# Kernel tuning notes

Hardware: AMD Instinct MI355X
Metric: run time of the kernel (lower is better)

## Reference

```python
import jax, jax.numpy as jnp
import numpy as np

D = 1024      # model_dim
H = 16        # num_attention_heads
HD = D // H   # head dim
FFN = 4096    # ffn_dim
EPS = 1e-5


def _mha(q_in, k_in, v_in, wq, bq, wk, bk, wv, bv):
    B, Sq, _ = q_in.shape
    Sk = k_in.shape[1]
    def split(x, S):
        return x.reshape(B, S, H, HD).transpose(0, 2, 1, 3)  # [B,H,S,HD]
    Q = split(q_in @ wq + bq, Sq)
    K = split(k_in @ wk + bk, Sk)
    V = split(v_in @ wv + bv, Sk)
    scores = jnp.einsum('bhqd,bhkd->bhqk', Q, K) / (HD ** 0.5)
    probs = jax.nn.softmax(scores, axis=-1)
    ctx = jnp.einsum('bhqk,bhkd->bhqd', probs, V)
    return ctx.transpose(0, 2, 1, 3).reshape(B, Sq, D)


def _ln(x, g, b):
    mu = jnp.mean(x, axis=-1, keepdims=True)
    var = jnp.mean(jnp.square(x - mu), axis=-1, keepdims=True)
    return (x - mu) * jax.lax.rsqrt(var + EPS) * g + b


def setup_inputs() -> dict:
    key = jax.random.key(0)
    ks = jax.random.split(key, 24)
    s = 1.0 / np.sqrt(D)
    inp = {
        'hidden_states': jax.random.normal(ks[0], (2, 2048, D), jnp.float32),
        'encoder_hidden_states': jax.random.normal(ks[1], (2, 2048, D), jnp.float32),
        # self-attention projections
        'sa_wq': jax.random.normal(ks[2], (D, D), jnp.float32) * s,
        'sa_bq': jnp.zeros((D,), jnp.float32),
        'sa_wk': jax.random.normal(ks[3], (D, D), jnp.float32) * s,
        'sa_bk': jnp.zeros((D,), jnp.float32),
        'sa_wv': jax.random.normal(ks[4], (D, D), jnp.float32) * s,
        'sa_bv': jnp.zeros((D,), jnp.float32),
        'ln1_g': jnp.ones((D,), jnp.float32),
        'ln1_b': jnp.zeros((D,), jnp.float32),
        # cross-attention projections
        'ca_wq': jax.random.normal(ks[5], (D, D), jnp.float32) * s,
        'ca_bq': jnp.zeros((D,), jnp.float32),
        'ca_wk': jax.random.normal(ks[6], (D, D), jnp.float32) * s,
        'ca_bk': jnp.zeros((D,), jnp.float32),
        'ca_wv': jax.random.normal(ks[7], (D, D), jnp.float32) * s,
        'ca_bv': jnp.zeros((D,), jnp.float32),
        'ln2_g': jnp.ones((D,), jnp.float32),
        'ln2_b': jnp.zeros((D,), jnp.float32),
        # feed-forward
        'fc1_w': jax.random.normal(ks[8], (D, FFN), jnp.float32) * s,
        'fc1_b': jnp.zeros((FFN,), jnp.float32),
        'fc2_w': jax.random.normal(ks[9], (FFN, D), jnp.float32) * (1.0 / np.sqrt(FFN)),
        'fc2_b': jnp.zeros((D,), jnp.float32),
        'ln3_g': jnp.ones((D,), jnp.float32),
        'ln3_b': jnp.zeros((D,), jnp.float32),
    }
    return inp


def reference(hidden_states, encoder_hidden_states,
              sa_wq, sa_bq, sa_wk, sa_bk, sa_wv, sa_bv, ln1_g, ln1_b,
              ca_wq, ca_bq, ca_wk, ca_bk, ca_wv, ca_bv, ln2_g, ln2_b,
              fc1_w, fc1_b, fc2_w, fc2_b, ln3_g, ln3_b):
    # self-attention + residual + LN  (dropout = identity in eval)
    h = _mha(hidden_states, hidden_states, hidden_states,
             sa_wq, sa_bq, sa_wk, sa_bk, sa_wv, sa_bv)
    x = _ln(hidden_states + h, ln1_g, ln1_b)
    # cross-attention + residual + LN
    h = _mha(x, encoder_hidden_states, encoder_hidden_states,
             ca_wq, ca_bq, ca_wk, ca_bk, ca_wv, ca_bv)
    x = _ln(x + h, ln2_g, ln2_b)
    # feed-forward + residual + LN
    h = jax.nn.relu(x @ fc1_w + fc1_b) @ fc2_w + fc2_b
    return _ln(x + h, ln3_g, ln3_b)
```

## Files before the change

kernel.cpp:

```cpp
#include <hip/hip_runtime.h>


typedef unsigned short u16;
typedef short v8s __attribute__((ext_vector_type(8)));
typedef float v4f __attribute__((ext_vector_type(4)));

#define LDP 72
#define LOG2E 1.44269504088896340736f

__device__ __forceinline__ float b2f(u16 h) {
    return __uint_as_float(((unsigned)h) << 16);
}
__device__ __forceinline__ u16 f2b(float f) {
    unsigned u = __float_as_uint(f);
    u += 0x7fffu + ((u >> 16) & 1u);
    return (u16)(u >> 16);
}
__device__ __forceinline__ u16 f2b_rz(float f) {
    return (u16)(__float_as_uint(f) >> 16);
}
__device__ __forceinline__ v8s pack8(const float* p) {
    float4 f0 = *(const float4*)p;
    float4 f1 = *(const float4*)(p + 4);
    v8s r;
    r[0] = (short)f2b(f0.x); r[1] = (short)f2b(f0.y);
    r[2] = (short)f2b(f0.z); r[3] = (short)f2b(f0.w);
    r[4] = (short)f2b(f1.x); r[5] = (short)f2b(f1.y);
    r[6] = (short)f2b(f1.z); r[7] = (short)f2b(f1.w);
    return r;
}
__device__ __forceinline__ void gload16(const void* g, void* l) {
    __builtin_amdgcn_global_load_lds(
        (const __attribute__((address_space(1))) unsigned int*)g,
        (__attribute__((address_space(3))) unsigned int*)l, 16, 0, 0);
}

__global__ __launch_bounds__(256) void transpose_f2b(
    const float* __restrict__ src, u16* __restrict__ dst, int R, int C)
{
    __shared__ u16 tile[32][33];
    const int t  = threadIdx.x;
    const int tx = t & 31, ty = t >> 5;
    const int r0 = blockIdx.y * 32, c0 = blockIdx.x * 32;
#pragma unroll
    for (int i = 0; i < 32; i += 8)
        tile[ty + i][tx] = f2b(src[(size_t)(r0 + ty + i) * C + c0 + tx]);
    __syncthreads();
#pragma unroll
    for (int i = 0; i < 32; i += 8)
        dst[(size_t)(c0 + ty + i) * R + r0 + tx] = tile[tx][ty + i];
}

__global__ __launch_bounds__(256) void prep_bias(
    const float* __restrict__ bq, const float* __restrict__ bk, const float* __restrict__ bv,
    const float* __restrict__ cbk, const float* __restrict__ cbv,
    float* __restrict__ sab, float* __restrict__ cakvb)
{
    int i = blockIdx.x * 256 + threadIdx.x;
    if (i < 1024) {
        sab[i]          = bq[i];
        sab[1024 + i]   = bk[i];
        sab[2048 + i]   = bv[i];
        cakvb[i]        = cbk[i];
        cakvb[1024 + i] = cbv[i];
    }
}

template <int AF32, int BN>
__global__ __launch_bounds__(256) void gemm_bt(
    const void* __restrict__ Ap, const u16* __restrict__ Bt,
    const float* __restrict__ bias, u16* __restrict__ C,
    int M, int N, int K, int relu, int qcols, float qscale,
    u16* __restrict__ vt, int vtcol0)
{
    constexpr int NI = BN / 32;
    __shared__ __align__(16) u16 Al[128 * 64];
    __shared__ __align__(16) u16 Bl[BN * 64];
    const int tid  = threadIdx.x;
    const int wave = tid >> 6, lane = tid & 63;
    const int quad = lane >> 4, tl = lane & 15;
    const int bm0 = blockIdx.y * 128, bn0 = blockIdx.x * BN;
    const int wm = (wave >> 1) * 64, wn = (wave & 1) * (BN / 2);
    const int srow = lane >> 3;
    const int scol = (((lane & 7) ^ srow) << 3);

    const v4f z4 = {0.f, 0.f, 0.f, 0.f};
    v4f acc[4][NI];
#pragma unroll
    for (int i = 0; i < 4; ++i)
#pragma unroll
        for (int j = 0; j < NI; ++j) acc[i][j] = z4;

    for (int kt = 0; kt < K; kt += 64) {
#pragma unroll
        for (int i = 0; i < 4; ++i) {
            const int c = wave * 4 + i;
            const int row = c * 8 + srow;
            if (AF32) {
                const float* Af = (const float*)Ap;
                *(v8s*)&Al[(size_t)row * 64 + scol] =
                    pack8(&Af[(size_t)(bm0 + row) * K + kt + ((lane & 7) << 3)]);
            } else {
                const u16* Ab = (const u16*)Ap;
                gload16(&Ab[(size_t)(bm0 + row) * K + kt + scol], &Al[c * 512]);
            }
        }
#pragma unroll
        for (int i = 0; i < NI; ++i) {
            const int c = wave * NI + i;
            const int row = c * 8 + srow;
            gload16(&Bt[(size_t)(bn0 + row) * K + kt + scol], &Bl[c * 512]);
        }
        __syncthreads();
#pragma unroll
        for (int kk = 0; kk < 2; ++kk) {
            const int pc = ((kk * 4 + quad) ^ (tl & 7)) << 3;
            v8s af[4], bf[NI];
#pragma unroll
            for (int i = 0; i < 4; ++i) af[i] = *(const v8s*)&Al[(wm + i * 16 + tl) * 64 + pc];
#pragma unroll
            for (int i = 0; i < NI; ++i) bf[i] = *(const v8s*)&Bl[(wn + i * 16 + tl) * 64 + pc];
#pragma unroll
            for (int mi = 0; mi < 4; ++mi)
#pragma unroll
                for (int ni = 0; ni < NI; ++ni)
                    acc[mi][ni] = __builtin_amdgcn_mfma_f32_16x16x32_bf16(
                        af[mi], bf[ni], acc[mi][ni], 0, 0, 0);
        }
        __syncthreads();
    }
#pragma unroll
    for (int ni = 0; ni < NI; ++ni) {
        int col = bn0 + wn + ni * 16 + tl;
        float bv = bias[col];
        if (vtcol0 >= 0 && col >= vtcol0) {
            int cv = col - vtcol0;
            int h = cv >> 6, hd = cv & 63;
#pragma unroll
            for (int mi = 0; mi < 4; ++mi) {
                int row0 = bm0 + wm + mi * 16 + (quad << 2);
                int bb = row0 >> 11, s = row0 & 2047;
                ushort4 pk;
                pk.x = f2b(acc[mi][ni][0] + bv);
                pk.y = f2b(acc[mi][ni][1] + bv);
                pk.z = f2b(acc[mi][ni][2] + bv);
                pk.w = f2b(acc[mi][ni][3] + bv);
                *(ushort4*)&vt[((size_t)(bb * 16 + h) * 64 + hd) * 2048 + s] = pk;
            }
        } else {
            float sc = (col < qcols) ? qscale : 1.0f;
#pragma unroll
            for (int mi = 0; mi < 4; ++mi) {
                int row0 = bm0 + wm + mi * 16 + (quad << 2);
#pragma unroll
                for (int r = 0; r < 4; ++r) {
                    float vv = acc[mi][ni][r] + bv;
                    if (relu) vv = fmaxf(vv, 0.f);
                    vv *= sc;
                    C[(size_t)(row0 + r) * N + col] = f2b(vv);
                }
            }
        }
    }
}

__global__ __launch_bounds__(256) void attn_v5(
    const u16* __restrict__ Q, int qs, const u16* __restrict__ Kp, int ks,
    const u16* __restrict__ Vt, u16* __restrict__ O, int os, int Sk)
{
    __shared__ __align__(16) u16 Kl[128 * 64];
    __shared__ __align__(16) u16 Vtl[64 * 128];
    __shared__ __align__(16) u16 Pl[4][32 * LDP];

    const int tid  = threadIdx.x;
    const int wave = tid >> 6, lane = tid & 63;
    const int quad = lane >> 4, tl = lane & 15;
    const int b = blockIdx.y >> 4, h = blockIdx.y & 15;
    const int srow = lane >> 3;
    const int scolK = (((lane & 7) ^ srow) << 3);
    const int vri = lane >> 4, vj = lane & 15;

    const u16* qb  = Q  + (size_t)(b * 2048) * qs + h * 64;
    const u16* kb  = Kp + (size_t)(b * 2048) * ks + h * 64;
    const u16* vtb = Vt + (size_t)blockIdx.y * 64 * 2048;
    u16*       ob  = O  + (size_t)(b * 2048) * os + h * 64;
    const int qr0 = blockIdx.x * 128 + wave * 32;

    v8s qf[2][2];
#pragma unroll
    for (int mi = 0; mi < 2; ++mi)
#pragma unroll
        for (int kk = 0; kk < 2; ++kk)
            qf[mi][kk] = *(const v8s*)&qb[(size_t)(qr0 + mi * 16 + tl) * qs + kk * 32 + quad * 8];

    const v4f z4 = {0.f, 0.f, 0.f, 0.f};
    v4f oacc[2][4] = {{z4, z4, z4, z4}, {z4, z4, z4, z4}};
    float l_part[2][4] = {{0.f, 0.f, 0.f, 0.f}, {0.f, 0.f, 0.f, 0.f}};
    u16* Pw = &Pl[wave][0];

    const int pc0 = (quad ^ (tl & 7)) << 3;
    const int pc1 = ((4 + quad) ^ (tl & 7)) << 3;

    for (int kt = 0; kt < Sk; kt += 128) {
#pragma unroll
        for (int i = 0; i < 4; ++i) {
            const int c = wave * 4 + i;
            const int row = c * 8 + srow;
            gload16(&kb[(size_t)(kt + row) * ks + scolK], &Kl[c * 512]);
        }
#pragma unroll
        for (int i = 0; i < 4; ++i) {
            const int c = wave * 4 + i;
            const int vr = c * 4 + vri;
            const int g = (vj & 8) | ((vj & 7) ^ (vr & 7));
            gload16(&vtb[(size_t)vr * 2048 + kt + (g << 3)], &Vtl[c * 512]);
        }
        __syncthreads();

#pragma unroll
        for (int hf = 0; hf < 2; ++hf) {
#pragma unroll
            for (int nt = 0; nt < 4; ++nt) {
                const int krow = ((hf * 4 + nt) * 16 + tl) * 64;
                v8s k0 = *(const v8s*)&Kl[krow + pc0];
                v8s k1 = *(const v8s*)&Kl[krow + pc1];
#pragma unroll
                for (int mi = 0; mi < 2; ++mi) {
                    v4f a = z4;
                    a = __builtin_amdgcn_mfma_f32_16x16x32_bf16(qf[mi][0], k0, a, 0, 0, 0);
                    a = __builtin_amdgcn_mfma_f32_16x16x32_bf16(qf[mi][1], k1, a, 0, 0, 0);
#pragma unroll
                    for (int r = 0; r < 4; ++r) {
                        float p = exp2f(a[r]);
                        l_part[mi][r] += p;
                        Pw[(mi * 16 + quad * 4 + r) * LDP + nt * 16 + tl] = f2b_rz(p);
                    }
                }
            }
            asm volatile("" ::: "memory");

            v8s pf[2][2];
#pragma unroll
            for (int mi = 0; mi < 2; ++mi) {
                pf[mi][0] = *(const v8s*)&Pw[(mi * 16 + tl) * LDP + quad * 8];
                pf[mi][1] = *(const v8s*)&Pw[(mi * 16 + tl) * LDP + 32 + quad * 8];
            }
            const int pv0 = ((hf * 8) | (quad ^ (tl & 7))) << 3;
            const int pv1 = ((hf * 8) | ((4 + quad) ^ (tl & 7))) << 3;
#pragma unroll
            for (int d = 0; d < 4; ++d) {
                const int vbase = (d * 16 + tl) * 128;
                v8s v0 = *(const v8s*)&Vtl[vbase + pv0];
                v8s v1 = *(const v8s*)&Vtl[vbase + pv1];
#pragma unroll
                for (int mi = 0; mi < 2; ++mi) {
                    oacc[mi][d] = __builtin_amdgcn_mfma_f32_16x16x32_bf16(pf[mi][0], v0, oacc[mi][d], 0, 0, 0);
                    oacc[mi][d] = __builtin_amdgcn_mfma_f32_16x16x32_bf16(pf[mi][1], v1, oacc[mi][d], 0, 0, 0);
                }
            }
            asm volatile("" ::: "memory");
        }
        __syncthreads();
    }

#pragma unroll
    for (int mi = 0; mi < 2; ++mi)
#pragma unroll
        for (int r = 0; r < 4; ++r) {
            float rs = l_part[mi][r];
            rs += __shfl_xor(rs, 1);
            rs += __shfl_xor(rs, 2);
            rs += __shfl_xor(rs, 4);
            rs += __shfl_xor(rs, 8);
            float inv = 1.0f / rs;
#pragma unroll
            for (int d = 0; d < 4; ++d)
                ob[(size_t)(qr0 + mi * 16 + quad * 4 + r) * os + d * 16 + tl] =
                    f2b(oacc[mi][d][r] * inv);
        }
}

template <int XF32, int OF32>
__global__ __launch_bounds__(256) void add_ln(
    const void* __restrict__ Xv, const u16* __restrict__ Hh,
    const float* __restrict__ G, const float* __restrict__ Bb,
    void* __restrict__ Outv)
{
    const int row = blockIdx.x, t = threadIdx.x;
    float v0, v1, v2, v3;
    {
        ushort4 hv = *(const ushort4*)&Hh[(size_t)row * 1024 + t * 4];
        if (XF32) {
            const float* xr = (const float*)Xv + (size_t)row * 1024;
            float4 xv = *(const float4*)&xr[t * 4];
            v0 = xv.x + b2f(hv.x); v1 = xv.y + b2f(hv.y);
            v2 = xv.z + b2f(hv.z); v3 = xv.w + b2f(hv.w);
        } else {
            const u16* xr = (const u16*)Xv + (size_t)row * 1024;
            ushort4 xv = *(const ushort4*)&xr[t * 4];
            v0 = b2f(xv.x) + b2f(hv.x); v1 = b2f(xv.y) + b2f(hv.y);
            v2 = b2f(xv.z) + b2f(hv.z); v3 = b2f(xv.w) + b2f(hv.w);
        }
    }

    float s1 = v0 + v1 + v2 + v3;
    float s2 = v0 * v0 + v1 * v1 + v2 * v2 + v3 * v3;
#pragma unroll
    for (int o = 1; o < 64; o <<= 1) {
        s1 += __shfl_xor(s1, o);
        s2 += __shfl_xor(s2, o);
    }
    __shared__ float red[8];
    const int wave = t >> 6, lane = t & 63;
    if (lane == 0) { red[wave] = s1; red[4 + wave] = s2; }
    __syncthreads();
    s1 = red[0] + red[1] + red[2] + red[3];
    s2 = red[4] + red[5] + red[6] + red[7];

    const float mu = s1 * (1.f / 1024.f);
    float var = s2 * (1.f / 1024.f) - mu * mu;
    var = fmaxf(var, 0.f);
    const float rs = rsqrtf(var + 1e-5f);

    float4 gv = *(const float4*)&G[t * 4];
    float4 bv = *(const float4*)&Bb[t * 4];
    float o0 = (v0 - mu) * rs * gv.x + bv.x;
    float o1 = (v1 - mu) * rs * gv.y + bv.y;
    float o2 = (v2 - mu) * rs * gv.z + bv.z;
    float o3 = (v3 - mu) * rs * gv.w + bv.w;

    if (OF32) {
        float4 ov = {o0, o1, o2, o3};
        *(float4*)&((float*)Outv)[(size_t)row * 1024 + t * 4] = ov;
    } else {
        ushort4 ov;
        ov.x = f2b(o0); ov.y = f2b(o1); ov.z = f2b(o2); ov.w = f2b(o3);
        *(ushort4*)&((u16*)Outv)[(size_t)row * 1024 + t * 4] = ov;
    }
}

extern "C" void kernel_launch(void* const* d_in, const int* in_sizes, int n_in,
                              void* d_out, int out_size, void* d_ws, size_t ws_size,
                              hipStream_t stream) {
    const float* x0  = (const float*)d_in[0];
    const float* enc = (const float*)d_in[1];

    char* wsb = (char*)d_ws;
    const size_t MB = 1024u * 1024u;
    u16*   wt_sa   = (u16*)(wsb);
    u16*   wt_caq  = (u16*)(wsb + 6  * MB);
    u16*   wt_cakv = (u16*)(wsb + 8  * MB);
    float* sab     = (float*)(wsb + 12 * MB);
    float* cakvb   = (float*)(wsb + 12 * MB + 16384);
    char*  arena   = wsb + 12 * MB + 32768;
    u16* QKV    = (u16*)(arena);
    u16* hbuf   = (u16*)(arena + 24 * MB);
    u16* x1     = (u16*)(arena + 32 * MB);
    u16* Vt     = (u16*)(arena + 40 * MB);
    u16* Q2     = (u16*)(arena);
    u16* KV2    = (u16*)(arena + 8  * MB);
    u16* x2     = (u16*)(arena);
    u16* wt_fc1 = (u16*)(wsb);
    u16* wt_fc2 = (u16*)(arena + 8  * MB);
    u16* tbuf   = (u16*)(arena + 16 * MB);
    u16* h3     = (u16*)(wsb);

    const float QSC = 0.125f * LOG2E;

    prep_bias<<<4, 256, 0, stream>>>(
        (const float*)d_in[3], (const float*)d_in[5], (const float*)d_in[7],
        (const float*)d_in[13], (const float*)d_in[15], sab, cakvb);

    transpose_f2b<<<dim3(32, 32), 256, 0, stream>>>((const float*)d_in[2],  wt_sa,               1024, 1024);
    transpose_f2b<<<dim3(32, 32), 256, 0, stream>>>((const float*)d_in[4],  wt_sa + 1024*1024,   1024, 1024);
    transpose_f2b<<<dim3(32, 32), 256, 0, stream>>>((const float*)d_in[6],  wt_sa + 2*1024*1024, 1024, 1024);
    transpose_f2b<<<dim3(32, 32), 256, 0, stream>>>((const float*)d_in[10], wt_caq,              1024, 1024);
    transpose_f2b<<<dim3(32, 32), 256, 0, stream>>>((const float*)d_in[12], wt_cakv,             1024, 1024);
    transpose_f2b<<<dim3(32, 32), 256, 0, stream>>>((const float*)d_in[14], wt_cakv + 1024*1024, 1024, 1024);

    gemm_bt<1, 128><<<dim3(24, 32), 256, 0, stream>>>(
        x0, wt_sa, sab, QKV, 4096, 3072, 1024, 0, 1024, QSC, Vt, 2048);
    attn_v5<<<dim3(16, 32), 256, 0, stream>>>(QKV, 3072, QKV + 1024, 3072, Vt, hbuf, 1024, 2048);
    add_ln<1, 0><<<4096, 256, 0, stream>>>(x0, hbuf, (const float*)d_in[8], (const float*)d_in[9], x1);

    gemm_bt<0, 64><<<dim3(16, 32), 256, 0, stream>>>(
        x1, wt_caq, (const float*)d_in[11], Q2, 4096, 1024, 1024, 0, 1024, QSC, (u16*)nullptr, -1);
    gemm_bt<1, 128><<<dim3(16, 32), 256, 0, stream>>>(
        enc, wt_cakv, cakvb, KV2, 4096, 2048, 1024, 0, 0, 1.0f, Vt, 1024);
    attn_v5<<<dim3(16, 32), 256, 0, stream>>>(Q2, 1024, KV2, 2048, Vt, hbuf, 1024, 2048);
    add_ln<0, 0><<<4096, 256, 0, stream>>>(x1, hbuf, (const float*)d_in[16], (const float*)d_in[17], x2);

    transpose_f2b<<<dim3(128, 32), 256, 0, stream>>>((const float*)d_in[18], wt_fc1, 1024, 4096);
    transpose_f2b<<<dim3(32, 128), 256, 0, stream>>>((const float*)d_in[20], wt_fc2, 4096, 1024);
    gemm_bt<0, 128><<<dim3(32, 32), 256, 0, stream>>>(
        x2, wt_fc1, (const float*)d_in[19], tbuf, 4096, 4096, 1024, 1, 0, 1.0f, (u16*)nullptr, -1);
    gemm_bt<0, 64><<<dim3(16, 32), 256, 0, stream>>>(
        tbuf, wt_fc2, (const float*)d_in[21], h3, 4096, 1024, 4096, 0, 0, 1.0f, (u16*)nullptr, -1);
    add_ln<0, 1><<<4096, 256, 0, stream>>>(x2, h3, (const float*)d_in[22], (const float*)d_in[23], d_out);
}
```

Measured before the change: 569.0 us.

## Pre-convert fp32 GEMM inputs to bf16 and transpose attention score MFMA

Adds a conv_f2b kernel that converts the fp32 hidden and encoder activations to bf16 up front. This lets every GEMM load A through the async global_load_lds path instead of doing fp32 loads and packing in the inner loop. In attention, the QK MFMA operands are swapped so each lane holds four consecutive keys for one query row. Those are packed into a single 8-byte P store, and the row-sum reduction drops from four shuffles per element to two shuffles per row. The cost is two extra conversion launches and extra bf16 buffer traffic, with the buffers reusing the hbuf arena region.

```diff
diff --git a/kernel.cpp b/kernel.cpp
--- a/kernel.cpp
+++ b/kernel.cpp
@@ -2,6 +2,7 @@
 
 
 typedef unsigned short u16;
+typedef unsigned int u32;
 typedef short v8s __attribute__((ext_vector_type(8)));
 typedef float v4f __attribute__((ext_vector_type(4)));
 
@@ -9,30 +10,33 @@
 #define LOG2E 1.44269504088896340736f
 
 __device__ __forceinline__ float b2f(u16 h) {
-    return __uint_as_float(((unsigned)h) << 16);
+    return __uint_as_float(((u32)h) << 16);
 }
 __device__ __forceinline__ u16 f2b(float f) {
-    unsigned u = __float_as_uint(f);
+    u32 u = __float_as_uint(f);
     u += 0x7fffu + ((u >> 16) & 1u);
     return (u16)(u >> 16);
 }
-__device__ __forceinline__ u16 f2b_rz(float f) {
-    return (u16)(__float_as_uint(f) >> 16);
-}
-__device__ __forceinline__ v8s pack8(const float* p) {
-    float4 f0 = *(const float4*)p;
-    float4 f1 = *(const float4*)(p + 4);
-    v8s r;
-    r[0] = (short)f2b(f0.x); r[1] = (short)f2b(f0.y);
-    r[2] = (short)f2b(f0.z); r[3] = (short)f2b(f0.w);
-    r[4] = (short)f2b(f1.x); r[5] = (short)f2b(f1.y);
-    r[6] = (short)f2b(f1.z); r[7] = (short)f2b(f1.w);
-    return r;
+__device__ __forceinline__ u32 pack2_rz(float lo, float hi) {
+    return (__float_as_uint(hi) & 0xffff0000u) | (__float_as_uint(lo) >> 16);
 }
 __device__ __forceinline__ void gload16(const void* g, void* l) {
     __builtin_amdgcn_global_load_lds(
         (const __attribute__((address_space(1))) unsigned int*)g,
         (__attribute__((address_space(3))) unsigned int*)l, 16, 0, 0);
+}
+
+__global__ __launch_bounds__(256) void conv_f2b(
+    const float* __restrict__ src, u16* __restrict__ dst)
+{
+    const size_t i = ((size_t)blockIdx.x * 256 + threadIdx.x) * 8;
+    float4 a = *(const float4*)&src[i];
+    float4 b = *(const float4*)&src[i + 4];
+    ushort4 o0, o1;
+    o0.x = f2b(a.x); o0.y = f2b(a.y); o0.z = f2b(a.z); o0.w = f2b(a.w);
+    o1.x = f2b(b.x); o1.y = f2b(b.y); o1.z = f2b(b.z); o1.w = f2b(b.w);
+    *(ushort4*)&dst[i] = o0;
+    *(ushort4*)&dst[i + 4] = o1;
 }
 
 __global__ __launch_bounds__(256) void transpose_f2b(
@@ -66,9 +70,9 @@
     }
 }
 
-template <int AF32, int BN>
+template <int BN>
 __global__ __launch_bounds__(256) void gemm_bt(
-    const void* __restrict__ Ap, const u16* __restrict__ Bt,
+    const u16* __restrict__ A, const u16* __restrict__ Bt,
     const float* __restrict__ bias, u16* __restrict__ C,
     int M, int N, int K, int relu, int qcols, float qscale,
     u16* __restrict__ vt, int vtcol0)
@@ -96,14 +100,7 @@
         for (int i = 0; i < 4; ++i) {
             const int c = wave * 4 + i;
             const int row = c * 8 + srow;
-            if (AF32) {
-                const float* Af = (const float*)Ap;
-                *(v8s*)&Al[(size_t)row * 64 + scol] =
-                    pack8(&Af[(size_t)(bm0 + row) * K + kt + ((lane & 7) << 3)]);
-            } else {
-                const u16* Ab = (const u16*)Ap;
-                gload16(&Ab[(size_t)(bm0 + row) * K + kt + scol], &Al[c * 512]);
-            }
+            gload16(&A[(size_t)(bm0 + row) * K + kt + scol], &Al[c * 512]);
         }
 #pragma unroll
         for (int i = 0; i < NI; ++i) {
@@ -164,7 +161,7 @@
     }
 }
 
-__global__ __launch_bounds__(256) void attn_v5(
+__global__ __launch_bounds__(256) void attn_v6(
     const u16* __restrict__ Q, int qs, const u16* __restrict__ Kp, int ks,
     const u16* __restrict__ Vt, u16* __restrict__ O, int os, int Sk)
 {
@@ -195,7 +192,7 @@
 
     const v4f z4 = {0.f, 0.f, 0.f, 0.f};
     v4f oacc[2][4] = {{z4, z4, z4, z4}, {z4, z4, z4, z4}};
-    float l_part[2][4] = {{0.f, 0.f, 0.f, 0.f}, {0.f, 0.f, 0.f, 0.f}};
+    float l_q[2] = {0.f, 0.f};
     u16* Pw = &Pl[wave][0];
 
     const int pc0 = (quad ^ (tl & 7)) << 3;
@@ -227,14 +224,15 @@
 #pragma unroll
                 for (int mi = 0; mi < 2; ++mi) {
                     v4f a = z4;
-                    a = __builtin_amdgcn_mfma_f32_16x16x32_bf16(qf[mi][0], k0, a, 0, 0, 0);
-                    a = __builtin_amdgcn_mfma_f32_16x16x32_bf16(qf[mi][1], k1, a, 0, 0, 0);
-#pragma unroll
-                    for (int r = 0; r < 4; ++r) {
-                        float p = exp2f(a[r]);
-                        l_part[mi][r] += p;
-                        Pw[(mi * 16 + quad * 4 + r) * LDP + nt * 16 + tl] = f2b_rz(p);
-                    }
+                    a = __builtin_amdgcn_mfma_f32_16x16x32_bf16(k0, qf[mi][0], a, 0, 0, 0);
+                    a = __builtin_amdgcn_mfma_f32_16x16x32_bf16(k1, qf[mi][1], a, 0, 0, 0);
+                    float p0 = exp2f(a[0]), p1 = exp2f(a[1]);
+                    float p2 = exp2f(a[2]), p3 = exp2f(a[3]);
+                    l_q[mi] += (p0 + p1) + (p2 + p3);
+                    uint2 pk;
+                    pk.x = pack2_rz(p0, p1);
+                    pk.y = pack2_rz(p2, p3);
+                    *(uint2*)&Pw[(mi * 16 + tl) * LDP + nt * 16 + quad * 4] = pk;
                 }
             }
             asm volatile("" ::: "memory");
@@ -264,15 +262,16 @@
     }
 
 #pragma unroll
+    for (int mi = 0; mi < 2; ++mi) {
+        l_q[mi] += __shfl_xor(l_q[mi], 16);
+        l_q[mi] += __shfl_xor(l_q[mi], 32);
+    }
+
+#pragma unroll
     for (int mi = 0; mi < 2; ++mi)
 #pragma unroll
         for (int r = 0; r < 4; ++r) {
-            float rs = l_part[mi][r];
-            rs += __shfl_xor(rs, 1);
-            rs += __shfl_xor(rs, 2);
-            rs += __shfl_xor(rs, 4);
-            rs += __shfl_xor(rs, 8);
-            float inv = 1.0f / rs;
+            float inv = 1.0f / __shfl(l_q[mi], quad * 4 + r);
 #pragma unroll
             for (int d = 0; d < 4; ++d)
                 ob[(size_t)(qr0 + mi * 16 + quad * 4 + r) * os + d * 16 + tl] =
@@ -355,6 +354,8 @@
     char*  arena   = wsb + 12 * MB + 32768;
     u16* QKV    = (u16*)(arena);
     u16* hbuf   = (u16*)(arena + 24 * MB);
+    u16* x0b    = (u16*)(arena + 24 * MB);
+    u16* encb   = (u16*)(arena + 24 * MB);
     u16* x1     = (u16*)(arena + 32 * MB);
     u16* Vt     = (u16*)(arena + 40 * MB);
     u16* Q2     = (u16*)(arena);
@@ -378,23 +379,25 @@
     transpose_f2b<<<dim3(32, 32), 256, 0, stream>>>((const float*)d_in[12], wt_cakv,             1024, 1024);
     transpose_f2b<<<dim3(32, 32), 256, 0, stream>>>((const float*)d_in[14], wt_cakv + 1024*1024, 1024, 1024);
 
-    gemm_bt<1, 128><<<dim3(24, 32), 256, 0, stream>>>(
-        x0, wt_sa, sab, QKV, 4096, 3072, 1024, 0, 1024, QSC, Vt, 2048);
-    attn_v5<<<dim3(16, 32), 256, 0, stream>>>(QKV, 3072, QKV + 1024, 3072, Vt, hbuf, 1024, 2048);
+    conv_f2b<<<2048, 256, 0, stream>>>(x0, x0b);
+    gemm_bt<128><<<dim3(24, 32), 256, 0, stream>>>(
+        x0b, wt_sa, sab, QKV, 4096, 3072, 1024, 0, 1024, QSC, Vt, 2048);
+    attn_v6<<<dim3(16, 32), 256, 0, stream>>>(QKV, 3072, QKV + 1024, 3072, Vt, hbuf, 1024, 2048);
     add_ln<1, 0><<<4096, 256, 0, stream>>>(x0, hbuf, (const float*)d_in[8], (const float*)d_in[9], x1);
 
-    gemm_bt<0, 64><<<dim3(16, 32), 256, 0, stream>>>(
+    conv_f2b<<<2048, 256, 0, stream>>>(enc, encb);
+    gemm_bt<64><<<dim3(16, 32), 256, 0, stream>>>(
         x1, wt_caq, (const float*)d_in[11], Q2, 4096, 1024, 1024, 0, 1024, QSC, (u16*)nullptr, -1);
-    gemm_bt<1, 128><<<dim3(16, 32), 256, 0, stream>>>(
-        enc, wt_cakv, cakvb, KV2, 4096, 2048, 1024, 0, 0, 1.0f, Vt, 1024);
-    attn_v5<<<dim3(16, 32), 256, 0, stream>>>(Q2, 1024, KV2, 2048, Vt, hbuf, 1024, 2048);
+    gemm_bt<128><<<dim3(16, 32), 256, 0, stream>>>(
+        encb, wt_cakv, cakvb, KV2, 4096, 2048, 1024, 0, 0, 1.0f, Vt, 1024);
+    attn_v6<<<dim3(16, 32), 256, 0, stream>>>(Q2, 1024, KV2, 2048, Vt, hbuf, 1024, 2048);
     add_ln<0, 0><<<4096, 256, 0, stream>>>(x1, hbuf, (const float*)d_in[16], (const float*)d_in[17], x2);
 
     transpose_f2b<<<dim3(128, 32), 256, 0, stream>>>((const float*)d_in[18], wt_fc1, 1024, 4096);
     transpose_f2b<<<dim3(32, 128), 256, 0, stream>>>((const float*)d_in[20], wt_fc2, 4096, 1024);
-    gemm_bt<0, 128><<<dim3(32, 32), 256, 0, stream>>>(
+    gemm_bt<128><<<dim3(32, 32), 256, 0, stream>>>(
         x2, wt_fc1, (const float*)d_in[19], tbuf, 4096, 4096, 1024, 1, 0, 1.0f, (u16*)nullptr, -1);
-    gemm_bt<0, 64><<<dim3(16, 32), 256, 0, stream>>>(
+    gemm_bt<64><<<dim3(16, 32), 256, 0, stream>>>(
         tbuf, wt_fc2, (const float*)d_in[21], h3, 4096, 1024, 4096, 0, 0, 1.0f, (u16*)nullptr, -1);
     add_ln<0, 1><<<4096, 256, 0, stream>>>(x2, h3, (const float*)d_in[22], (const float*)d_in[23], d_out);
 }
```

Measured after the change: 531.8 us. 6.5% less time.
